# Kernel optimization log

Measured on AMD Instinct MI355X. Metric: run time of the kernel, lower is better.

Reference implementation:

```python
import jax, jax.numpy as jnp
import numpy as np

TOP_K = 2
EPS = 1e-6


def setup_inputs() -> dict:
    key = jax.random.key(0)
    ks = jax.random.split(key, 8)
    B, S, D, E = 4, 2048, 2048, 8
    sd = 1.0 / np.sqrt(D)
    return {
        "x": jax.random.normal(ks[0], (B, S, D), dtype=jnp.float32),
        "Wr": jax.random.normal(ks[1], (D, E), dtype=jnp.float32) * sd,
        "br": jnp.zeros((E,), dtype=jnp.float32),
        "We": jax.random.normal(ks[2], (E, D, D), dtype=jnp.float32) * sd,
        "be": jnp.zeros((E, D), dtype=jnp.float32),
        "Wo": jax.random.normal(ks[3], (D, D), dtype=jnp.float32) * sd,
        "bo": jnp.zeros((D,), dtype=jnp.float32),
        "norm_w": jnp.ones((D,), dtype=jnp.float32),
    }


def reference(x, Wr, br, We, be, Wo, bo, norm_w):
    B, S, D = x.shape
    xf = x.reshape(-1, D)  # [T, D]
    # Router + top-k gating (softmax over the k selected logits, as in source)
    logits = xf @ Wr + br                      # [T, E]
    vals, idx = jax.lax.top_k(logits, TOP_K)   # [T, K]
    gates = jax.nn.softmax(vals, axis=-1)      # [T, K]
    # Expert FFN: Linear -> SiLU (dropout=0 -> identity). Dense over all experts,
    # then gather the top-k outputs per token.
    all_out = jax.nn.silu(jnp.einsum('td,edf->tef', xf, We) + be)  # [T, E, D]
    picked = jnp.take_along_axis(all_out, idx[:, :, None], axis=1)  # [T, K, D]
    combined = jnp.sum(gates[:, :, None] * picked, axis=1)          # [T, D]
    out = combined @ Wo + bo
    y = xf + out
    rms = jnp.sqrt(jnp.mean(y * y, axis=-1, keepdims=True) + EPS)
    return (norm_w * (y / rms)).reshape(B, S, D)
```

## Files before the change

### kernel.cpp

```cpp
#include <hip/hip_runtime.h>
#include <hip/hip_bf16.h>
#include <stdint.h>

typedef __bf16 bf16;
typedef __bf16 bf16x4 __attribute__((ext_vector_type(4)));
typedef __bf16 bf16x8 __attribute__((ext_vector_type(8)));
typedef float floatx4 __attribute__((ext_vector_type(4)));

#define T_TOK 8192
#define DIM 2048
#define NE 8
#define MAX_CHUNKS 136

__device__ inline void gld_lds16(const bf16* g, bf16* l) {
  __builtin_amdgcn_global_load_lds(
      (const __attribute__((address_space(1))) uint32_t*)g,
      (__attribute__((address_space(3))) uint32_t*)l, 16, 0, 0);
}

__global__ __launch_bounds__(256) void transpose_convert(
    const float* __restrict__ in, bf16* __restrict__ out) {
  __shared__ float tile[32][33];
  const int tx = threadIdx.x & 31;
  const int ty = threadIdx.x >> 5;
  const int n0 = blockIdx.x * 32;
  const int k0 = blockIdx.y * 32;
  const size_t base = (size_t)blockIdx.z * DIM * DIM;
  const float* src = in + base;
  bf16* dst = out + base;
#pragma unroll
  for (int i = 0; i < 32; i += 8)
    tile[ty + i][tx] = src[(size_t)(k0 + ty + i) * DIM + n0 + tx];
  __syncthreads();
#pragma unroll
  for (int i = 0; i < 32; i += 8)
    dst[(size_t)(n0 + ty + i) * DIM + k0 + tx] = (bf16)tile[tx][ty + i];
}

__global__ __launch_bounds__(256) void router_kernel(
    const float* __restrict__ x, const float* __restrict__ Wr,
    const float* __restrict__ br, int* __restrict__ cnt,
    int* __restrict__ aid_list, float* __restrict__ gate_list,
    bf16* __restrict__ xb) {
  const int t = blockIdx.x;
  const int tid = threadIdx.x;
  const float* xr = x + (size_t)t * DIM;
  bf16* xbr = xb + (size_t)t * DIM;
  float acc[8];
#pragma unroll
  for (int e = 0; e < 8; ++e) acc[e] = 0.f;
#pragma unroll
  for (int h = 0; h < 2; ++h) {
    const int d0 = tid * 4 + h * 1024;
    float4 xv = *(const float4*)&xr[d0];
    bf16x4 xc;
    xc[0] = (bf16)xv.x; xc[1] = (bf16)xv.y; xc[2] = (bf16)xv.z; xc[3] = (bf16)xv.w;
    *(bf16x4*)&xbr[d0] = xc;
    const float* wp = &Wr[(size_t)d0 * NE];
    float xe[4] = {xv.x, xv.y, xv.z, xv.w};
#pragma unroll
    for (int q = 0; q < 4; ++q) {
      float4 w0 = *(const float4*)&wp[q * 8];
      float4 w1 = *(const float4*)&wp[q * 8 + 4];
      acc[0] += xe[q] * w0.x; acc[1] += xe[q] * w0.y;
      acc[2] += xe[q] * w0.z; acc[3] += xe[q] * w0.w;
      acc[4] += xe[q] * w1.x; acc[5] += xe[q] * w1.y;
      acc[6] += xe[q] * w1.z; acc[7] += xe[q] * w1.w;
    }
  }
#pragma unroll
  for (int e = 0; e < 8; ++e) {
#pragma unroll
    for (int off = 32; off > 0; off >>= 1) acc[e] += __shfl_down(acc[e], off, 64);
  }
  __shared__ float red[4][8];
  const int lane = tid & 63, wid = tid >> 6;
  if (lane == 0) {
#pragma unroll
    for (int e = 0; e < 8; ++e) red[wid][e] = acc[e];
  }
  __syncthreads();
  if (tid == 0) {
    float lg[8];
#pragma unroll
    for (int e = 0; e < 8; ++e)
      lg[e] = red[0][e] + red[1][e] + red[2][e] + red[3][e] + br[e];
    int i0 = 0;
#pragma unroll
    for (int e = 1; e < 8; ++e) if (lg[e] > lg[i0]) i0 = e;
    int i1 = (i0 == 0) ? 1 : 0;
#pragma unroll
    for (int e = 0; e < 8; ++e)
      if (e != i0 && lg[e] > lg[i1]) i1 = e;
    const float g0 = 1.f / (1.f + expf(lg[i1] - lg[i0]));
    const float g1 = 1.f - g0;
    int p0 = atomicAdd(&cnt[i0], 1);
    aid_list[i0 * T_TOK + p0] = t * 2;
    gate_list[i0 * T_TOK + p0] = g0;
    int p1 = atomicAdd(&cnt[i1], 1);
    aid_list[i1 * T_TOK + p1] = t * 2 + 1;
    gate_list[i1 * T_TOK + p1] = g1;
  }
}

__global__ void build_chunks(const int* __restrict__ cnt, int2* __restrict__ chunks,
                             int* __restrict__ nchunks) {
  if (threadIdx.x == 0 && blockIdx.x == 0) {
    int tot = 0;
#pragma unroll
    for (int e = 0; e < NE; ++e) {
      const int ne = cnt[e];
      for (int m0 = 0; m0 < ne; m0 += 128) chunks[tot++] = make_int2(e, m0);
    }
    *nchunks = tot;
  }
}


__global__ __launch_bounds__(256, 2) void expert_gemm(
    const bf16* __restrict__ xb, const bf16* __restrict__ Wt,
    const float* __restrict__ be, const int* __restrict__ cnt,
    const int* __restrict__ aid_list, const float* __restrict__ gate_list,
    const int2* __restrict__ chunks, const int* __restrict__ nchunks,
    bf16* __restrict__ aout) {
  const int cid = blockIdx.x;
  if (cid >= *nchunks) return;
  const int2 ch = chunks[cid];
  const int e = ch.x;
  const int m0 = ch.y;
  const int ne = cnt[e];
  const int n0 = blockIdx.y * 128;
  const int tid = threadIdx.x;

  __shared__ bf16 As[128][64];
  __shared__ bf16 Bs[128][64];
  __shared__ int aidS[128];
  __shared__ float gateS[128];

  if (tid < 128) {
    const int idx = m0 + tid;
    aidS[tid] = (idx < ne) ? aid_list[e * T_TOK + idx] : 0;
    gateS[tid] = (idx < ne) ? gate_list[e * T_TOK + idx] : 0.f;
  }
  __syncthreads();

  const int r0 = tid >> 3;
  const int kq = (((tid & 7) ^ (r0 & 7))) * 8;
  const bf16* wbase = Wt + (size_t)e * DIM * DIM;
  const bf16* ap[4];
  const bf16* bp[4];
#pragma unroll
  for (int h = 0; h < 4; ++h) {
    const int r = r0 + 32 * h;
    ap[h] = xb + (size_t)(aidS[r] >> 1) * DIM + kq;
    bp[h] = wbase + (size_t)(n0 + r) * DIM + kq;
  }
  bf16* const asF = &As[0][0];
  bf16* const bsF = &Bs[0][0];

  const int lane = tid & 63, wid = tid >> 6;
  const int wr = (wid >> 1) * 64, wc = (wid & 1) * 64;
  const int quad = lane >> 4, l15 = lane & 15;

  floatx4 acc[4][4];
#pragma unroll
  for (int i = 0; i < 4; ++i)
#pragma unroll
    for (int j = 0; j < 4; ++j) acc[i][j] = (floatx4){0.f, 0.f, 0.f, 0.f};

  int aoff[2][4], boff[2][4];
#pragma unroll
  for (int s = 0; s < 2; ++s) {
    const int kb = s * 4 + quad;
#pragma unroll
    for (int i = 0; i < 4; ++i) {
      const int mi = wr + i * 16 + l15;
      aoff[s][i] = mi * 64 + ((kb ^ (mi & 7)) * 8);
      const int nj = wc + i * 16 + l15;
      boff[s][i] = nj * 64 + ((kb ^ (nj & 7)) * 8);
    }
  }

  for (int k0 = 0; k0 < DIM; k0 += 64) {
#pragma unroll
    for (int h = 0; h < 4; ++h) {
      gld_lds16(bp[h] + k0, bsF + ((size_t)tid + 256 * h) * 8);
      gld_lds16(ap[h] + k0, asF + ((size_t)tid + 256 * h) * 8);
    }
    __syncthreads();

#pragma unroll
    for (int s = 0; s < 2; ++s) {
      bf16x8 af[4], bfr[4];
#pragma unroll
      for (int i = 0; i < 4; ++i) af[i] = *(const bf16x8*)&asF[aoff[s][i]];
#pragma unroll
      for (int j = 0; j < 4; ++j) bfr[j] = *(const bf16x8*)&bsF[boff[s][j]];
#pragma unroll
      for (int i = 0; i < 4; ++i)
#pragma unroll
        for (int j = 0; j < 4; ++j)
          acc[i][j] = __builtin_amdgcn_mfma_f32_16x16x32_bf16(af[i], bfr[j], acc[i][j], 0, 0, 0);
    }
    __syncthreads();
  }

#pragma unroll
  for (int j = 0; j < 4; ++j) {
    const int col = n0 + wc + j * 16 + l15;
    const float bev = be[e * DIM + col];
#pragma unroll
    for (int i = 0; i < 4; ++i) {
#pragma unroll
      for (int r = 0; r < 4; ++r) {
        const int rl = wr + i * 16 + quad * 4 + r;
        if (m0 + rl < ne) {
          float v = acc[i][j][r] + bev;
          v = v / (1.f + __expf(-v));
          v *= gateS[rl];
          aout[(size_t)aidS[rl] * DIM + col] = (bf16)v;
        }
      }
    }
  }
}

__global__ __launch_bounds__(256) void combine_kernel(
    const bf16* __restrict__ aout, bf16* __restrict__ hcomb) {
  const size_t i = ((size_t)blockIdx.x * 256 + threadIdx.x) * 8;
  const size_t row = i >> 11;
  const size_t d = i & 2047;
  const bf16* a0 = aout + (row << 12) + d;
  bf16x8 u0 = *(const bf16x8*)a0;
  bf16x8 u1 = *(const bf16x8*)(a0 + DIM);
  bf16x8 s;
#pragma unroll
  for (int q = 0; q < 8; ++q) s[q] = (bf16)((float)u0[q] + (float)u1[q]);
  *(bf16x8*)&hcomb[i] = s;
}

__global__ __launch_bounds__(256, 2) void proj_gemm(
    const bf16* __restrict__ hcomb, const bf16* __restrict__ Wot,
    const float* __restrict__ bo, const float* __restrict__ x,
    float* __restrict__ y) {
  const int m0 = blockIdx.x * 128;
  const int n0 = blockIdx.y * 128;
  const int tid = threadIdx.x;

  __shared__ bf16 As[128][64];
  __shared__ bf16 Bs[128][64];

  const int r0 = tid >> 3;
  const int kq = (((tid & 7) ^ (r0 & 7))) * 8;
  const bf16* ap[4];
  const bf16* bp[4];
#pragma unroll
  for (int h = 0; h < 4; ++h) {
    const int r = r0 + 32 * h;
    ap[h] = hcomb + (size_t)(m0 + r) * DIM + kq;
    bp[h] = Wot + (size_t)(n0 + r) * DIM + kq;
  }
  bf16* const asF = &As[0][0];
  bf16* const bsF = &Bs[0][0];

  const int lane = tid & 63, wid = tid >> 6;
  const int wr = (wid >> 1) * 64, wc = (wid & 1) * 64;
  const int quad = lane >> 4, l15 = lane & 15;

  floatx4 acc[4][4];
#pragma unroll
  for (int i = 0; i < 4; ++i)
#pragma unroll
    for (int j = 0; j < 4; ++j) acc[i][j] = (floatx4){0.f, 0.f, 0.f, 0.f};

  int aoff[2][4], boff[2][4];
#pragma unroll
  for (int s = 0; s < 2; ++s) {
    const int kb = s * 4 + quad;
#pragma unroll
    for (int i = 0; i < 4; ++i) {
      const int mi = wr + i * 16 + l15;
      aoff[s][i] = mi * 64 + ((kb ^ (mi & 7)) * 8);
      const int nj = wc + i * 16 + l15;
      boff[s][i] = nj * 64 + ((kb ^ (nj & 7)) * 8);
    }
  }

  for (int k0 = 0; k0 < DIM; k0 += 64) {
#pragma unroll
    for (int h = 0; h < 4; ++h) {
      gld_lds16(bp[h] + k0, bsF + ((size_t)tid + 256 * h) * 8);
      gld_lds16(ap[h] + k0, asF + ((size_t)tid + 256 * h) * 8);
    }
    __syncthreads();

#pragma unroll
    for (int s = 0; s < 2; ++s) {
      bf16x8 af[4], bfr[4];
#pragma unroll
      for (int i = 0; i < 4; ++i) af[i] = *(const bf16x8*)&asF[aoff[s][i]];
#pragma unroll
      for (int j = 0; j < 4; ++j) bfr[j] = *(const bf16x8*)&bsF[boff[s][j]];
#pragma unroll
      for (int i = 0; i < 4; ++i)
#pragma unroll
        for (int j = 0; j < 4; ++j)
          acc[i][j] = __builtin_amdgcn_mfma_f32_16x16x32_bf16(af[i], bfr[j], acc[i][j], 0, 0, 0);
    }
    __syncthreads();
  }

#pragma unroll
  for (int j = 0; j < 4; ++j) {
    const int col = n0 + wc + j * 16 + l15;
    const float bov = bo[col];
#pragma unroll
    for (int i = 0; i < 4; ++i) {
#pragma unroll
      for (int r = 0; r < 4; ++r) {
        const int rl = wr + i * 16 + quad * 4 + r;
        const size_t o = (size_t)(m0 + rl) * DIM + col;
        y[o] = acc[i][j][r] + bov + x[o];
      }
    }
  }
}

__global__ __launch_bounds__(256) void rmsnorm_kernel(
    float* __restrict__ y, const float* __restrict__ w) {
  const int row = blockIdx.x;
  const int tid = threadIdx.x;
  float* yr = y + (size_t)row * DIM;
  float4 v0 = ((const float4*)yr)[tid];
  float4 v1 = ((const float4*)yr)[tid + 256];
  float ss = v0.x * v0.x + v0.y * v0.y + v0.z * v0.z + v0.w * v0.w +
             v1.x * v1.x + v1.y * v1.y + v1.z * v1.z + v1.w * v1.w;
#pragma unroll
  for (int off = 32; off > 0; off >>= 1) ss += __shfl_down(ss, off, 64);
  __shared__ float s4[4];
  const int lane = tid & 63, wid = tid >> 6;
  if (lane == 0) s4[wid] = ss;
  __syncthreads();
  const float tot = s4[0] + s4[1] + s4[2] + s4[3];
  const float r = rsqrtf(tot / (float)DIM + 1e-6f);
  float4 w0 = ((const float4*)w)[tid];
  float4 w1 = ((const float4*)w)[tid + 256];
  float4 o0 = make_float4(v0.x * r * w0.x, v0.y * r * w0.y, v0.z * r * w0.z, v0.w * r * w0.w);
  float4 o1 = make_float4(v1.x * r * w1.x, v1.y * r * w1.y, v1.z * r * w1.z, v1.w * r * w1.w);
  ((float4*)yr)[tid] = o0;
  ((float4*)yr)[tid + 256] = o1;
}

extern "C" void kernel_launch(void* const* d_in, const int* in_sizes, int n_in,
                              void* d_out, int out_size, void* d_ws, size_t ws_size,
                              hipStream_t stream) {
  const float* x  = (const float*)d_in[0];
  const float* Wr = (const float*)d_in[1];
  const float* br = (const float*)d_in[2];
  const float* We = (const float*)d_in[3];
  const float* be = (const float*)d_in[4];
  const float* Wo = (const float*)d_in[5];
  const float* bo = (const float*)d_in[6];
  const float* nw = (const float*)d_in[7];
  float* out = (float*)d_out;

  uint8_t* ws = (uint8_t*)d_ws;
  size_t off = 0;
  auto carve = [&](size_t bytes) -> void* {
    void* p = ws + off;
    off += (bytes + 255) & ~(size_t)255;
    return p;
  };
  int*   cnt       = (int*)carve(NE * sizeof(int));
  int*   aid_list  = (int*)carve((size_t)NE * T_TOK * sizeof(int));
  float* gate_list = (float*)carve((size_t)NE * T_TOK * sizeof(float));
  int2*  chunks    = (int2*)carve(MAX_CHUNKS * sizeof(int2));
  int*   nchunks   = (int*)carve(sizeof(int));
  bf16*  We_t      = (bf16*)carve((size_t)NE * DIM * DIM * sizeof(bf16));
  bf16*  Wo_t      = (bf16*)carve((size_t)DIM * DIM * sizeof(bf16));
  bf16*  aoutb     = (bf16*)carve((size_t)T_TOK * 2 * DIM * sizeof(bf16));
  bf16*  xb        = (bf16*)carve((size_t)T_TOK * DIM * sizeof(bf16));
  bf16*  hcomb     = We_t;
  (void)ws_size; (void)in_sizes; (void)n_in; (void)out_size;

  hipMemsetAsync(cnt, 0, NE * sizeof(int), stream);
  transpose_convert<<<dim3(DIM / 32, DIM / 32, NE), 256, 0, stream>>>(We, We_t);
  transpose_convert<<<dim3(DIM / 32, DIM / 32, 1), 256, 0, stream>>>(Wo, Wo_t);
  router_kernel<<<T_TOK, 256, 0, stream>>>(x, Wr, br, cnt, aid_list, gate_list, xb);
  build_chunks<<<1, 64, 0, stream>>>(cnt, chunks, nchunks);
  expert_gemm<<<dim3(MAX_CHUNKS, DIM / 128), 256, 0, stream>>>(
      xb, We_t, be, cnt, aid_list, gate_list, chunks, nchunks, aoutb);
  combine_kernel<<<(T_TOK * DIM / 8) / 256, 256, 0, stream>>>(aoutb, hcomb);
  proj_gemm<<<dim3(T_TOK / 128, DIM / 128), 256, 0, stream>>>(hcomb, Wo_t, bo, x, out);
  rmsnorm_kernel<<<T_TOK, 256, 0, stream>>>(out, nw);
}
```

Before: 838.9 us.

## Double-buffer LDS tiles in expert and projection GEMMs; merge and vectorize weight transpose

```diff
diff --git a/kernel.cpp b/kernel.cpp
--- a/kernel.cpp
+++ b/kernel.cpp
@@ -19,22 +19,32 @@
 }
 
 __global__ __launch_bounds__(256) void transpose_convert(
-    const float* __restrict__ in, bf16* __restrict__ out) {
-  __shared__ float tile[32][33];
-  const int tx = threadIdx.x & 31;
-  const int ty = threadIdx.x >> 5;
-  const int n0 = blockIdx.x * 32;
-  const int k0 = blockIdx.y * 32;
-  const size_t base = (size_t)blockIdx.z * DIM * DIM;
-  const float* src = in + base;
-  bf16* dst = out + base;
-#pragma unroll
-  for (int i = 0; i < 32; i += 8)
-    tile[ty + i][tx] = src[(size_t)(k0 + ty + i) * DIM + n0 + tx];
+    const float* __restrict__ We, const float* __restrict__ Wo,
+    bf16* __restrict__ We_t, bf16* __restrict__ Wo_t) {
+  const int z = blockIdx.z;
+  const float* src = (z < NE) ? We + (size_t)z * DIM * DIM : Wo;
+  bf16* dst = (z < NE) ? We_t + (size_t)z * DIM * DIM : Wo_t;
+  __shared__ float tile[64][65];
+  const int n0 = blockIdx.x * 64, k0 = blockIdx.y * 64;
+  const int tid = threadIdx.x;
+  const int lr = tid >> 4;
+  const int lc = (tid & 15) * 4;
+#pragma unroll
+  for (int i = 0; i < 64; i += 16) {
+    float4 v = *(const float4*)&src[(size_t)(k0 + lr + i) * DIM + n0 + lc];
+    tile[lr + i][lc] = v.x; tile[lr + i][lc + 1] = v.y;
+    tile[lr + i][lc + 2] = v.z; tile[lr + i][lc + 3] = v.w;
+  }
   __syncthreads();
-#pragma unroll
-  for (int i = 0; i < 32; i += 8)
-    dst[(size_t)(n0 + ty + i) * DIM + k0 + tx] = (bf16)tile[tx][ty + i];
+  const int sr = tid >> 3;
+  const int sc = (tid & 7) * 8;
+#pragma unroll
+  for (int i = 0; i < 64; i += 32) {
+    bf16x8 o;
+#pragma unroll
+    for (int j = 0; j < 8; ++j) o[j] = (bf16)tile[sc + j][sr + i];
+    *(bf16x8*)&dst[(size_t)(n0 + sr + i) * DIM + k0 + sc] = o;
+  }
 }
 
 __global__ __launch_bounds__(256) void router_kernel(
@@ -132,8 +142,8 @@
   const int n0 = blockIdx.y * 128;
   const int tid = threadIdx.x;
 
-  __shared__ bf16 As[128][64];
-  __shared__ bf16 Bs[128][64];
+  __shared__ bf16 As[2][128 * 64];
+  __shared__ bf16 Bs[2][128 * 64];
   __shared__ int aidS[128];
   __shared__ float gateS[128];
 
@@ -155,8 +165,6 @@
     ap[h] = xb + (size_t)(aidS[r] >> 1) * DIM + kq;
     bp[h] = wbase + (size_t)(n0 + r) * DIM + kq;
   }
-  bf16* const asF = &As[0][0];
-  bf16* const bsF = &Bs[0][0];
 
   const int lane = tid & 63, wid = tid >> 6;
   const int wr = (wid >> 1) * 64, wc = (wid & 1) * 64;
@@ -181,28 +189,37 @@
     }
   }
 
+#pragma unroll
+  for (int h = 0; h < 4; ++h) {
+    gld_lds16(bp[h], &Bs[0][((size_t)tid + 256 * h) * 8]);
+    gld_lds16(ap[h], &As[0][((size_t)tid + 256 * h) * 8]);
+  }
+
+  int buf = 0;
   for (int k0 = 0; k0 < DIM; k0 += 64) {
-#pragma unroll
-    for (int h = 0; h < 4; ++h) {
-      gld_lds16(bp[h] + k0, bsF + ((size_t)tid + 256 * h) * 8);
-      gld_lds16(ap[h] + k0, asF + ((size_t)tid + 256 * h) * 8);
-    }
     __syncthreads();
-
+    if (k0 + 64 < DIM) {
+      const int nb = buf ^ 1;
+#pragma unroll
+      for (int h = 0; h < 4; ++h) {
+        gld_lds16(bp[h] + k0 + 64, &Bs[nb][((size_t)tid + 256 * h) * 8]);
+        gld_lds16(ap[h] + k0 + 64, &As[nb][((size_t)tid + 256 * h) * 8]);
+      }
+    }
 #pragma unroll
     for (int s = 0; s < 2; ++s) {
       bf16x8 af[4], bfr[4];
 #pragma unroll
-      for (int i = 0; i < 4; ++i) af[i] = *(const bf16x8*)&asF[aoff[s][i]];
-#pragma unroll
-      for (int j = 0; j < 4; ++j) bfr[j] = *(const bf16x8*)&bsF[boff[s][j]];
+      for (int i = 0; i < 4; ++i) af[i] = *(const bf16x8*)&As[buf][aoff[s][i]];
+#pragma unroll
+      for (int j = 0; j < 4; ++j) bfr[j] = *(const bf16x8*)&Bs[buf][boff[s][j]];
 #pragma unroll
       for (int i = 0; i < 4; ++i)
 #pragma unroll
         for (int j = 0; j < 4; ++j)
           acc[i][j] = __builtin_amdgcn_mfma_f32_16x16x32_bf16(af[i], bfr[j], acc[i][j], 0, 0, 0);
     }
-    __syncthreads();
+    buf ^= 1;
   }
 
 #pragma unroll
@@ -247,8 +264,8 @@
   const int n0 = blockIdx.y * 128;
   const int tid = threadIdx.x;
 
-  __shared__ bf16 As[128][64];
-  __shared__ bf16 Bs[128][64];
+  __shared__ bf16 As[2][128 * 64];
+  __shared__ bf16 Bs[2][128 * 64];
 
   const int r0 = tid >> 3;
   const int kq = (((tid & 7) ^ (r0 & 7))) * 8;
@@ -260,8 +277,6 @@
     ap[h] = hcomb + (size_t)(m0 + r) * DIM + kq;
     bp[h] = Wot + (size_t)(n0 + r) * DIM + kq;
   }
-  bf16* const asF = &As[0][0];
-  bf16* const bsF = &Bs[0][0];
 
   const int lane = tid & 63, wid = tid >> 6;
   const int wr = (wid >> 1) * 64, wc = (wid & 1) * 64;
@@ -286,28 +301,37 @@
     }
   }
 
+#pragma unroll
+  for (int h = 0; h < 4; ++h) {
+    gld_lds16(bp[h], &Bs[0][((size_t)tid + 256 * h) * 8]);
+    gld_lds16(ap[h], &As[0][((size_t)tid + 256 * h) * 8]);
+  }
+
+  int buf = 0;
   for (int k0 = 0; k0 < DIM; k0 += 64) {
-#pragma unroll
-    for (int h = 0; h < 4; ++h) {
-      gld_lds16(bp[h] + k0, bsF + ((size_t)tid + 256 * h) * 8);
-      gld_lds16(ap[h] + k0, asF + ((size_t)tid + 256 * h) * 8);
-    }
     __syncthreads();
-
+    if (k0 + 64 < DIM) {
+      const int nb = buf ^ 1;
+#pragma unroll
+      for (int h = 0; h < 4; ++h) {
+        gld_lds16(bp[h] + k0 + 64, &Bs[nb][((size_t)tid + 256 * h) * 8]);
+        gld_lds16(ap[h] + k0 + 64, &As[nb][((size_t)tid + 256 * h) * 8]);
+      }
+    }
 #pragma unroll
     for (int s = 0; s < 2; ++s) {
       bf16x8 af[4], bfr[4];
 #pragma unroll
-      for (int i = 0; i < 4; ++i) af[i] = *(const bf16x8*)&asF[aoff[s][i]];
-#pragma unroll
-      for (int j = 0; j < 4; ++j) bfr[j] = *(const bf16x8*)&bsF[boff[s][j]];
+      for (int i = 0; i < 4; ++i) af[i] = *(const bf16x8*)&As[buf][aoff[s][i]];
+#pragma unroll
+      for (int j = 0; j < 4; ++j) bfr[j] = *(const bf16x8*)&Bs[buf][boff[s][j]];
 #pragma unroll
       for (int i = 0; i < 4; ++i)
 #pragma unroll
         for (int j = 0; j < 4; ++j)
           acc[i][j] = __builtin_amdgcn_mfma_f32_16x16x32_bf16(af[i], bfr[j], acc[i][j], 0, 0, 0);
     }
-    __syncthreads();
+    buf ^= 1;
   }
 
 #pragma unroll
@@ -384,8 +408,7 @@
   (void)ws_size; (void)in_sizes; (void)n_in; (void)out_size;
 
   hipMemsetAsync(cnt, 0, NE * sizeof(int), stream);
-  transpose_convert<<<dim3(DIM / 32, DIM / 32, NE), 256, 0, stream>>>(We, We_t);
-  transpose_convert<<<dim3(DIM / 32, DIM / 32, 1), 256, 0, stream>>>(Wo, Wo_t);
+  transpose_convert<<<dim3(DIM / 64, DIM / 64, NE + 1), 256, 0, stream>>>(We, Wo, We_t, Wo_t);
   router_kernel<<<T_TOK, 256, 0, stream>>>(x, Wr, br, cnt, aid_list, gate_list, xb);
   build_chunks<<<1, 64, 0, stream>>>(cnt, chunks, nchunks);
   expert_gemm<<<dim3(MAX_CHUNKS, DIM / 128), 256, 0, stream>>>(
```

After: 867.5 us. 1.03x slower.
